# Performance work log

Measured on AMD Instinct MI355X. Metric: run time of the kernel, lower is better.

Reference implementation:

```python
import jax, jax.numpy as jnp
import numpy as np

HIDDEN = 128
HEADS = 8
HEAD_DIM = HIDDEN // HEADS
N_NODES = 100000
N_EDGES = 1600000


def setup_inputs() -> dict:
    key = jax.random.key(0)
    ks = jax.random.split(key, 12)
    s = 1.0 / np.sqrt(HIDDEN)
    inp = {
        "x": jax.random.normal(ks[0], (N_NODES, HIDDEN), dtype=jnp.float32),
        "edge_index": jax.random.randint(ks[1], (2, N_EDGES), 0, N_NODES, dtype=jnp.int32),
        "edge_emb": jax.random.normal(ks[2], (N_EDGES, HIDDEN), dtype=jnp.float32),
        "q_w": jax.random.uniform(ks[3], (HIDDEN, HIDDEN), jnp.float32, -s, s),
        "q_b": jax.random.uniform(ks[4], (HIDDEN,), jnp.float32, -s, s),
        "k_w": jax.random.uniform(ks[5], (HIDDEN, HIDDEN), jnp.float32, -s, s),
        "k_b": jax.random.uniform(ks[6], (HIDDEN,), jnp.float32, -s, s),
        "v_w": jax.random.uniform(ks[7], (HIDDEN, HIDDEN), jnp.float32, -s, s),
        "v_b": jax.random.uniform(ks[8], (HIDDEN,), jnp.float32, -s, s),
        "out_w": jax.random.uniform(ks[9], (HIDDEN, HIDDEN), jnp.float32, -s, s),
        "out_b": jax.random.uniform(ks[10], (HIDDEN,), jnp.float32, -s, s),
        "eb_w": jax.random.uniform(ks[11], (HEADS, HIDDEN), jnp.float32, -s, s),
        "eb_b": jnp.zeros((HEADS,), dtype=jnp.float32),
    }
    return inp


def reference(x, edge_index, edge_emb, q_w, q_b, k_w, k_b, v_w, v_b, out_w, out_b, eb_w, eb_b):
    n = x.shape[0]
    # node projections -> [N, H, D]
    q = (x @ q_w.T + q_b).reshape(n, HEADS, HEAD_DIM)
    k = (x @ k_w.T + k_b).reshape(n, HEADS, HEAD_DIM)
    v = (x @ v_w.T + v_b).reshape(n, HEADS, HEAD_DIM)

    row, col = edge_index[0], edge_index[1]
    # per-edge scores: [E, H]
    scores = jnp.einsum('ehd,ehd->eh', q[row], k[col]) / jnp.sqrt(jnp.float32(HEAD_DIM))
    scores = scores + edge_emb @ eb_w.T + eb_b

    # segmented softmax over incoming edges of each destination node `row`
    seg_max = jax.ops.segment_max(scores, row, num_segments=n)  # [N, H]
    exp_scores = jnp.exp(scores - seg_max[row])
    seg_sum = jax.ops.segment_sum(exp_scores, row, num_segments=n)  # [N, H]
    attn = exp_scores / (seg_sum[row] + 1e-10)  # [E, H]

    # weighted scatter-aggregation of values
    weighted_v = attn[..., None] * v[col]  # [E, H, D]
    out = jax.ops.segment_sum(weighted_v, row, num_segments=n)  # [N, H, D]
    out = out.reshape(n, HIDDEN)
    return out @ out_w.T + out_b
```

## Files before the change

kernel.cpp:

```cpp
#include <hip/hip_runtime.h>

#define HID 128
#define NH 8

typedef __attribute__((ext_vector_type(8))) short short8;
typedef __attribute__((ext_vector_type(4))) float f32x4;

__device__ __forceinline__ float dot4f(float4 a, float4 b) {
    return a.x*b.x + a.y*b.y + a.z*b.z + a.w*b.w;
}
__device__ __forceinline__ unsigned short f2bf(float f) {
    unsigned int u = __float_as_uint(f);
    u = (u + 0x7FFF + ((u >> 16) & 1)) >> 16;
    return (unsigned short)u;
}
__device__ __forceinline__ float bf2f(unsigned short s) {
    return __uint_as_float((unsigned int)s << 16);
}

__global__ void k_hist(const int* __restrict__ row, int E, int* __restrict__ count) {
    int i = blockIdx.x * blockDim.x + threadIdx.x;
    int stride = gridDim.x * blockDim.x;
    for (; i < E; i += stride) atomicAdd(&count[row[i]], 1);
}

__global__ void k_scan1(const int* __restrict__ in, int total,
                        int* __restrict__ out, int* __restrict__ bsums) {
    __shared__ int sd[256];
    int t = threadIdx.x;
    int base = blockIdx.x * 1024 + t * 4;
    int v0 = (base + 0 < total) ? in[base + 0] : 0;
    int v1 = (base + 1 < total) ? in[base + 1] : 0;
    int v2 = (base + 2 < total) ? in[base + 2] : 0;
    int v3 = (base + 3 < total) ? in[base + 3] : 0;
    int s = v0 + v1 + v2 + v3;
    sd[t] = s; __syncthreads();
    for (int off = 1; off < 256; off <<= 1) {
        int xx = (t >= off) ? sd[t - off] : 0;
        __syncthreads();
        sd[t] += xx;
        __syncthreads();
    }
    int excl = sd[t] - s;
    if (t == 255) bsums[blockIdx.x] = sd[255];
    int run = excl;
    if (base + 0 < total) out[base + 0] = run; run += v0;
    if (base + 1 < total) out[base + 1] = run; run += v1;
    if (base + 2 < total) out[base + 2] = run; run += v2;
    if (base + 3 < total) out[base + 3] = run;
}

__global__ void k_scan2(int* __restrict__ bs, int nb) {
    __shared__ int sd[128];
    int t = threadIdx.x;
    int vv = (t < nb) ? bs[t] : 0;
    sd[t] = vv; __syncthreads();
    for (int off = 1; off < 128; off <<= 1) {
        int xx = (t >= off) ? sd[t - off] : 0;
        __syncthreads();
        sd[t] += xx;
        __syncthreads();
    }
    if (t < nb) bs[t] = sd[t] - vv;
}

__global__ void k_scan3(int* __restrict__ out, int total, const int* __restrict__ bs) {
    int add = bs[blockIdx.x];
    int base = blockIdx.x * 1024 + threadIdx.x * 4;
    #pragma unroll
    for (int i = 0; i < 4; ++i)
        if (base + i < total) out[base + i] += add;
}

__global__ void k_scatter(const int* __restrict__ row, const int* __restrict__ col, int E,
                          const int* __restrict__ start, int* __restrict__ cursor,
                          int* __restrict__ pos, int* __restrict__ col_sorted) {
    int i = blockIdx.x * blockDim.x + threadIdx.x;
    int stride = gridDim.x * blockDim.x;
    for (; i < E; i += stride) {
        int r = row[i];
        int p = start[r] + atomicAdd(&cursor[r], 1);
        pos[i] = p;
        col_sorted[p] = col[i];
    }
}

__global__ void k_cvtw(const float* __restrict__ qw, const float* __restrict__ kw,
                       const float* __restrict__ vw, const float* __restrict__ ow,
                       unsigned short* __restrict__ wbf) {
    int i = blockIdx.x * 256 + threadIdx.x;
    int idx = i * 4;
    int m = idx >> 14;
    int off = idx & 16383;
    const float* src = (m == 0) ? qw : (m == 1) ? kw : (m == 2) ? vw : ow;
    float4 v = *(const float4*)(src + off);
    ushort4 o;
    o.x = f2bf(v.x); o.y = f2bf(v.y); o.z = f2bf(v.z); o.w = f2bf(v.w);
    *(ushort4*)(wbf + idx) = o;
}

__global__ __launch_bounds__(256) void k_qkv_mfma(
    const float* __restrict__ x, const unsigned short* __restrict__ wbf,
    const float* __restrict__ qb, const float* __restrict__ kb, const float* __restrict__ vb,
    unsigned short* __restrict__ qkvbf, int n)
{
    __shared__ unsigned short xs[64][136];
    int t = threadIdx.x;
    int m0 = blockIdx.x * 64;
    #pragma unroll
    for (int p = 0; p < 2; ++p) {
        int f = p * 256 + t;
        int r = f >> 3;
        int c16 = (f & 7) * 16;
        int node = m0 + r;
        float4 u0 = {0,0,0,0}, u1 = {0,0,0,0}, u2 = {0,0,0,0}, u3 = {0,0,0,0};
        if (node < n) {
            const float4* px = (const float4*)(x + (size_t)node * HID + c16);
            u0 = px[0]; u1 = px[1]; u2 = px[2]; u3 = px[3];
        }
        union { unsigned short u[8]; short8 v; } a, b;
        a.u[0]=f2bf(u0.x); a.u[1]=f2bf(u0.y); a.u[2]=f2bf(u0.z); a.u[3]=f2bf(u0.w);
        a.u[4]=f2bf(u1.x); a.u[5]=f2bf(u1.y); a.u[6]=f2bf(u1.z); a.u[7]=f2bf(u1.w);
        b.u[0]=f2bf(u2.x); b.u[1]=f2bf(u2.y); b.u[2]=f2bf(u2.z); b.u[3]=f2bf(u2.w);
        b.u[4]=f2bf(u3.x); b.u[5]=f2bf(u3.y); b.u[6]=f2bf(u3.z); b.u[7]=f2bf(u3.w);
        *(short8*)&xs[r][c16]     = a.v;
        *(short8*)&xs[r][c16 + 8] = b.v;
    }
    __syncthreads();

    int w = t >> 6, l = t & 63;
    int lr = l & 15, lc = l >> 4;
    short8 afr[4];
    #pragma unroll
    for (int c = 0; c < 4; ++c)
        afr[c] = *(const short8*)&xs[w * 16 + lr][c * 32 + lc * 8];

    #pragma unroll
    for (int m = 0; m < 3; ++m) {
        const float* bias = (m == 0) ? qb : (m == 1) ? kb : vb;
        #pragma unroll
        for (int ct = 0; ct < 8; ++ct) {
            int colg = ct * 16 + lr;
            f32x4 acc = {0.f, 0.f, 0.f, 0.f};
            const unsigned short* wrow = wbf + (size_t)m * 16384 + (size_t)colg * 128 + lc * 8;
            #pragma unroll
            for (int c = 0; c < 4; ++c) {
                short8 bfr = *(const short8*)(wrow + c * 32);
                acc = __builtin_amdgcn_mfma_f32_16x16x32_bf16(afr[c], bfr, acc, 0, 0, 0);
            }
            float bv = bias[colg];
            #pragma unroll
            for (int r = 0; r < 4; ++r) {
                int node = m0 + w * 16 + lc * 4 + r;
                if (node < n)
                    qkvbf[(size_t)node * 384 + m * 128 + colg] = f2bf(acc[r] + bv);
            }
        }
    }
}

__global__ __launch_bounds__(256) void k_ebias(
    const float* __restrict__ emb, const float* __restrict__ ebw,
    const float* __restrict__ ebb, const int* __restrict__ pos,
    float* __restrict__ out, int E)
{
    __shared__ float Es[32][132];
    __shared__ float Ws[8][132];
    int e0 = blockIdx.x * 32;
    int t = threadIdx.x;
    #pragma unroll
    for (int p = 0; p < 4; ++p) {
        int f = p * 256 + t;
        int r = f >> 5, c4 = (f & 31) * 4;
        float4 val = make_float4(0.f, 0.f, 0.f, 0.f);
        if (e0 + r < E) val = *(const float4*)(emb + (size_t)(e0 + r) * HID + c4);
        *(float4*)&Es[r][c4] = val;
    }
    {
        int r = t >> 5, c4 = (t & 31) * 4;
        *(float4*)&Ws[r][c4] = *(const float4*)(ebw + (size_t)r * HID + c4);
    }
    __syncthreads();
    int el = t >> 3, h = t & 7;
    float acc = 0.f;
    for (int c4 = 0; c4 < HID; c4 += 4) {
        float4 ev = *(const float4*)&Es[el][c4];
        float4 wv = *(const float4*)&Ws[h][c4];
        acc += dot4f(ev, wv);
    }
    int e = e0 + el;
    if (e < E) out[(size_t)pos[e] * NH + h] = acc + ebb[h];
}

__global__ __launch_bounds__(256) void k_attn(
    const unsigned short* __restrict__ qkvbf, const float* __restrict__ ebs,
    const int* __restrict__ cols, const int* __restrict__ start,
    float* __restrict__ out, int n, int E)
{
    int node = blockIdx.x * 4 + (threadIdx.x >> 6);
    if (node >= n) return;
    int l = threadIdx.x & 63;
    int slot = l >> 4, j = l & 15;
    int s0 = start[node];
    int deg = start[node + 1] - s0;

    float qf[8];
    {
        short8 qv = *(const short8*)(qkvbf + (size_t)node * 384 + j * 8);
        #pragma unroll
        for (int i = 0; i < 8; ++i) qf[i] = bf2f((unsigned short)qv[i]);
    }
    int colv = 0;
    if (l < deg && s0 + l < E) colv = cols[s0 + l];

    float acc[8] = {0.f,0.f,0.f,0.f,0.f,0.f,0.f,0.f};
    float denom = 0.f;

    for (int base = 0; base < deg; base += 4) {
        int idx = base + slot;
        bool act = idx < deg;
        int c = (idx < 64) ? __shfl(colv, idx) : (act ? cols[s0 + idx] : 0);
        const unsigned short* kv = qkvbf + (size_t)c * 384 + 128 + j * 8;
        short8 kk = *(const short8*)kv;
        short8 vv = *(const short8*)(kv + 128);
        float part = 0.f;
        #pragma unroll
        for (int i = 0; i < 8; ++i) part += qf[i] * bf2f((unsigned short)kk[i]);
        part += __shfl_xor(part, 1);
        float eb = act ? ebs[(size_t)(s0 + idx) * NH + (j >> 1)] : 0.f;
        float sc = part * 0.25f + eb;
        float es = act ? __expf(sc) : 0.f;
        denom += es;
        #pragma unroll
        for (int i = 0; i < 8; ++i) acc[i] += es * bf2f((unsigned short)vv[i]);
    }
    #pragma unroll
    for (int off = 16; off < 64; off <<= 1) {
        denom += __shfl_xor(denom, off);
        #pragma unroll
        for (int i = 0; i < 8; ++i) acc[i] += __shfl_xor(acc[i], off);
    }
    if (slot == 0) {
        float inv = 1.f / (denom + 1e-10f);
        float4 o0 = make_float4(acc[0]*inv, acc[1]*inv, acc[2]*inv, acc[3]*inv);
        float4 o1 = make_float4(acc[4]*inv, acc[5]*inv, acc[6]*inv, acc[7]*inv);
        *(float4*)(out + (size_t)node * HID + j * 8)     = o0;
        *(float4*)(out + (size_t)node * HID + j * 8 + 4) = o1;
    }
}

__global__ __launch_bounds__(256) void k_outproj_mfma(
    float* __restrict__ io, const unsigned short* __restrict__ wbf,
    const float* __restrict__ ob, int n)
{
    __shared__ unsigned short hs[64][136];
    int t = threadIdx.x;
    int m0 = blockIdx.x * 64;
    #pragma unroll
    for (int p = 0; p < 2; ++p) {
        int f = p * 256 + t;
        int r = f >> 3;
        int c16 = (f & 7) * 16;
        int node = m0 + r;
        float4 u0 = {0,0,0,0}, u1 = {0,0,0,0}, u2 = {0,0,0,0}, u3 = {0,0,0,0};
        if (node < n) {
            const float4* px = (const float4*)(io + (size_t)node * HID + c16);
            u0 = px[0]; u1 = px[1]; u2 = px[2]; u3 = px[3];
        }
        union { unsigned short u[8]; short8 v; } a, b;
        a.u[0]=f2bf(u0.x); a.u[1]=f2bf(u0.y); a.u[2]=f2bf(u0.z); a.u[3]=f2bf(u0.w);
        a.u[4]=f2bf(u1.x); a.u[5]=f2bf(u1.y); a.u[6]=f2bf(u1.z); a.u[7]=f2bf(u1.w);
        b.u[0]=f2bf(u2.x); b.u[1]=f2bf(u2.y); b.u[2]=f2bf(u2.z); b.u[3]=f2bf(u2.w);
        b.u[4]=f2bf(u3.x); b.u[5]=f2bf(u3.y); b.u[6]=f2bf(u3.z); b.u[7]=f2bf(u3.w);
        *(short8*)&hs[r][c16]     = a.v;
        *(short8*)&hs[r][c16 + 8] = b.v;
    }
    __syncthreads();

    int w = t >> 6, l = t & 63;
    int lr = l & 15, lc = l >> 4;
    short8 afr[4];
    #pragma unroll
    for (int c = 0; c < 4; ++c)
        afr[c] = *(const short8*)&hs[w * 16 + lr][c * 32 + lc * 8];

    #pragma unroll
    for (int ct = 0; ct < 8; ++ct) {
        int colg = ct * 16 + lr;
        f32x4 acc = {0.f, 0.f, 0.f, 0.f};
        const unsigned short* wrow = wbf + (size_t)3 * 16384 + (size_t)colg * 128 + lc * 8;
        #pragma unroll
        for (int c = 0; c < 4; ++c) {
            short8 bfr = *(const short8*)(wrow + c * 32);
            acc = __builtin_amdgcn_mfma_f32_16x16x32_bf16(afr[c], bfr, acc, 0, 0, 0);
        }
        float bv = ob[colg];
        #pragma unroll
        for (int r = 0; r < 4; ++r) {
            int node = m0 + w * 16 + lc * 4 + r;
            if (node < n)
                io[(size_t)node * HID + colg] = acc[r] + bv;
        }
    }
}

extern "C" void kernel_launch(void* const* d_in, const int* in_sizes, int n_in,
                              void* d_out, int out_size, void* d_ws, size_t ws_size,
                              hipStream_t stream) {
    const float* x   = (const float*)d_in[0];
    const int*   eix = (const int*)  d_in[1];
    const float* emb = (const float*)d_in[2];
    const float* qw  = (const float*)d_in[3];
    const float* qb  = (const float*)d_in[4];
    const float* kw  = (const float*)d_in[5];
    const float* kb  = (const float*)d_in[6];
    const float* vw  = (const float*)d_in[7];
    const float* vb  = (const float*)d_in[8];
    const float* ow  = (const float*)d_in[9];
    const float* ob  = (const float*)d_in[10];
    const float* ebw = (const float*)d_in[11];
    const float* ebb = (const float*)d_in[12];

    int n = in_sizes[0] / HID;
    int E = in_sizes[2] / HID;
    const int* row = eix;
    const int* col = eix + E;

    char* wsp = (char*)d_ws;
    auto alloc = [&](size_t bytes) -> void* {
        void* p = (void*)wsp;
        wsp += (bytes + 255) & ~(size_t)255;
        return p;
    };
    unsigned short* qkvbf = (unsigned short*)alloc((size_t)n * 384 * 2);
    unsigned short* wbf   = (unsigned short*)alloc((size_t)4 * 16384 * 2);
    float* ebias_s        = (float*)alloc((size_t)E * NH * 4);
    int* count            = (int*)alloc((size_t)(n + 2) * 4);
    int* startp           = (int*)alloc((size_t)(n + 2) * 4);
    int* bsums            = (int*)alloc(256 * 4);
    int* cursor           = (int*)alloc((size_t)n * 4);
    int* pos              = (int*)alloc((size_t)E * 4);
    int* col_sorted       = (int*)alloc((size_t)E * 4);

    hipMemsetAsync(count, 0, (size_t)(n + 1) * sizeof(int), stream);
    hipMemsetAsync(cursor, 0, (size_t)n * sizeof(int), stream);

    k_cvtw<<<64, 256, 0, stream>>>(qw, kw, vw, ow, wbf);
    k_hist<<<1024, 256, 0, stream>>>(row, E, count);

    int total = n + 1;
    int nb = (total + 1023) / 1024;
    k_scan1<<<nb, 256, 0, stream>>>(count, total, startp, bsums);
    k_scan2<<<1, 128, 0, stream>>>(bsums, nb);
    k_scan3<<<nb, 256, 0, stream>>>(startp, total, bsums);

    k_scatter<<<1024, 256, 0, stream>>>(row, col, E, startp, cursor, pos, col_sorted);

    k_qkv_mfma<<<(n + 63) / 64, 256, 0, stream>>>(x, wbf, qb, kb, vb, qkvbf, n);
    k_ebias<<<(E + 31) / 32, 256, 0, stream>>>(emb, ebw, ebb, pos, ebias_s, E);
    k_attn<<<(n + 3) / 4, 256, 0, stream>>>(qkvbf, ebias_s, col_sorted, startp,
                                            (float*)d_out, n, E);
    k_outproj_mfma<<<(n + 63) / 64, 256, 0, stream>>>((float*)d_out, wbf, ob, n);
}
```

Before: 628.7 us.

## Fuse edge-bias projection into CSR scatter kernel, dropping pos array

Merges the CSR scatter pass with the edge-embedding bias projection into one grid-stride kernel. Each group of 8 lanes reduces one edge's 128-wide embedding against all 8 head weights using shuffles. One lane claims the sorted slot with an atomic and broadcasts it, so the bias is written directly to its sorted position. This removes the separate ebias launch and the pos array write and read, and also doubles the grid size for hist. The risk is lower arithmetic efficiency from the shuffle reductions, and the 512 MB embedding stream now competes with the atomics.

Result: faster. 570.5 us (-9.3%).

```diff
diff --git a/kernel.cpp b/kernel.cpp
--- a/kernel.cpp
+++ b/kernel.cpp
@@ -6,9 +6,6 @@
 typedef __attribute__((ext_vector_type(8))) short short8;
 typedef __attribute__((ext_vector_type(4))) float f32x4;
 
-__device__ __forceinline__ float dot4f(float4 a, float4 b) {
-    return a.x*b.x + a.y*b.y + a.z*b.z + a.w*b.w;
-}
 __device__ __forceinline__ unsigned short f2bf(float f) {
     unsigned int u = __float_as_uint(f);
     u = (u + 0x7FFF + ((u >> 16) & 1)) >> 16;
@@ -72,16 +69,58 @@
         if (base + i < total) out[base + i] += add;
 }
 
-__global__ void k_scatter(const int* __restrict__ row, const int* __restrict__ col, int E,
-                          const int* __restrict__ start, int* __restrict__ cursor,
-                          int* __restrict__ pos, int* __restrict__ col_sorted) {
-    int i = blockIdx.x * blockDim.x + threadIdx.x;
-    int stride = gridDim.x * blockDim.x;
-    for (; i < E; i += stride) {
-        int r = row[i];
-        int p = start[r] + atomicAdd(&cursor[r], 1);
-        pos[i] = p;
-        col_sorted[p] = col[i];
+__global__ __launch_bounds__(256) void k_edge_fused(
+    const int* __restrict__ row, const int* __restrict__ col,
+    const float* __restrict__ emb, const float* __restrict__ ebw,
+    const float* __restrict__ ebb, const int* __restrict__ start,
+    int* __restrict__ cursor, int* __restrict__ col_sorted,
+    float* __restrict__ ebias_s, int E)
+{
+    __shared__ float Wx[8][4][8][4];
+    __shared__ float bb[8];
+    int t = threadIdx.x;
+    for (int i = t; i < 1024; i += 256) {
+        int j = i & 3, g = (i >> 2) & 7, c = (i >> 5) & 3, h = i >> 7;
+        Wx[h][c][g][j] = ebw[h * 128 + g * 16 + c * 4 + j];
+    }
+    if (t < 8) bb[t] = ebb[t];
+    __syncthreads();
+
+    int l = t & 63;
+    int g = l & 7;
+    int sub = l >> 3;
+    int wid = blockIdx.x * 4 + (t >> 6);
+    int nwaves = gridDim.x * 4;
+
+    for (int base = wid * 8; base < E; base += nwaves * 8) {
+        int e = base + sub;
+        bool act = e < E;
+        float p[8] = {0.f,0.f,0.f,0.f,0.f,0.f,0.f,0.f};
+        if (act) {
+            const float4* pe = (const float4*)(emb + (size_t)e * HID + g * 16);
+            #pragma unroll
+            for (int c = 0; c < 4; ++c) {
+                float4 ev = pe[c];
+                #pragma unroll
+                for (int h = 0; h < 8; ++h) {
+                    float4 wv = *(const float4*)&Wx[h][c][g][0];
+                    p[h] += ev.x*wv.x + ev.y*wv.y + ev.z*wv.z + ev.w*wv.w;
+                }
+            }
+        }
+        #pragma unroll
+        for (int off = 1; off < 8; off <<= 1) {
+            #pragma unroll
+            for (int h = 0; h < 8; ++h) p[h] += __shfl_xor(p[h], off);
+        }
+        int pslot = 0;
+        if (act && g == 0) {
+            int r = row[e];
+            pslot = start[r] + atomicAdd(&cursor[r], 1);
+            col_sorted[pslot] = col[e];
+        }
+        pslot = __shfl(pslot, l & 56);
+        if (act) ebias_s[(size_t)pslot * NH + g] = p[g] + bb[g];
     }
 }
 
@@ -159,39 +198,6 @@
     }
 }
 
-__global__ __launch_bounds__(256) void k_ebias(
-    const float* __restrict__ emb, const float* __restrict__ ebw,
-    const float* __restrict__ ebb, const int* __restrict__ pos,
-    float* __restrict__ out, int E)
-{
-    __shared__ float Es[32][132];
-    __shared__ float Ws[8][132];
-    int e0 = blockIdx.x * 32;
-    int t = threadIdx.x;
-    #pragma unroll
-    for (int p = 0; p < 4; ++p) {
-        int f = p * 256 + t;
-        int r = f >> 5, c4 = (f & 31) * 4;
-        float4 val = make_float4(0.f, 0.f, 0.f, 0.f);
-        if (e0 + r < E) val = *(const float4*)(emb + (size_t)(e0 + r) * HID + c4);
-        *(float4*)&Es[r][c4] = val;
-    }
-    {
-        int r = t >> 5, c4 = (t & 31) * 4;
-        *(float4*)&Ws[r][c4] = *(const float4*)(ebw + (size_t)r * HID + c4);
-    }
-    __syncthreads();
-    int el = t >> 3, h = t & 7;
-    float acc = 0.f;
-    for (int c4 = 0; c4 < HID; c4 += 4) {
-        float4 ev = *(const float4*)&Es[el][c4];
-        float4 wv = *(const float4*)&Ws[h][c4];
-        acc += dot4f(ev, wv);
-    }
-    int e = e0 + el;
-    if (e < E) out[(size_t)pos[e] * NH + h] = acc + ebb[h];
-}
-
 __global__ __launch_bounds__(256) void k_attn(
     const unsigned short* __restrict__ qkvbf, const float* __restrict__ ebs,
     const int* __restrict__ cols, const int* __restrict__ start,
@@ -211,7 +217,7 @@
         for (int i = 0; i < 8; ++i) qf[i] = bf2f((unsigned short)qv[i]);
     }
     int colv = 0;
-    if (l < deg && s0 + l < E) colv = cols[s0 + l];
+    if (l < deg) colv = cols[s0 + l];
 
     float acc[8] = {0.f,0.f,0.f,0.f,0.f,0.f,0.f,0.f};
     float denom = 0.f;
@@ -339,14 +345,13 @@
     int* startp           = (int*)alloc((size_t)(n + 2) * 4);
     int* bsums            = (int*)alloc(256 * 4);
     int* cursor           = (int*)alloc((size_t)n * 4);
-    int* pos              = (int*)alloc((size_t)E * 4);
     int* col_sorted       = (int*)alloc((size_t)E * 4);
 
     hipMemsetAsync(count, 0, (size_t)(n + 1) * sizeof(int), stream);
     hipMemsetAsync(cursor, 0, (size_t)n * sizeof(int), stream);
 
     k_cvtw<<<64, 256, 0, stream>>>(qw, kw, vw, ow, wbf);
-    k_hist<<<1024, 256, 0, stream>>>(row, E, count);
+    k_hist<<<2048, 256, 0, stream>>>(row, E, count);
 
     int total = n + 1;
     int nb = (total + 1023) / 1024;
@@ -354,10 +359,10 @@
     k_scan2<<<1, 128, 0, stream>>>(bsums, nb);
     k_scan3<<<nb, 256, 0, stream>>>(startp, total, bsums);
 
-    k_scatter<<<1024, 256, 0, stream>>>(row, col, E, startp, cursor, pos, col_sorted);
+    k_edge_fused<<<2048, 256, 0, stream>>>(row, col, emb, ebw, ebb, startp,
+                                           cursor, col_sorted, ebias_s, E);
 
     k_qkv_mfma<<<(n + 63) / 64, 256, 0, stream>>>(x, wbf, qb, kb, vb, qkvbf, n);
-    k_ebias<<<(E + 31) / 32, 256, 0, stream>>>(emb, ebw, ebb, pos, ebias_s, E);
     k_attn<<<(n + 3) / 4, 256, 0, stream>>>(qkvbf, ebias_s, col_sorted, startp,
                                             (float*)d_out, n, E);
     k_outproj_mfma<<<(n + 63) / 64, 256, 0, stream>>>((float*)d_out, wbf, ob, n);
```
